# Optimization experiments

Measured on AMD Instinct MI355X. Metric: run time of the kernel, lower is better.

The kernel has to match this reference:

```python
import jax, jax.numpy as jnp
import numpy as np

EMB = 768
NH = 12
DH = EMB // NH
NORM = float(np.sqrt(DH))  # 8.0


def setup_inputs() -> dict:
    key = jax.random.key(0)
    ks = jax.random.split(key, 9)
    B, S = 1, 4096
    s = 0.02  # realistic init scale for weights
    return {
        "x": jax.random.normal(ks[0], (B, S, EMB), jnp.float32),
        "mask": jnp.ones((B, S), jnp.float32),
        "Wq": jax.random.normal(ks[1], (EMB, EMB), jnp.float32) * s,
        "bq": jnp.zeros((EMB,), jnp.float32),
        "Wk": jax.random.normal(ks[2], (EMB, EMB), jnp.float32) * s,
        "bk": jnp.zeros((EMB,), jnp.float32),
        "Wv": jax.random.normal(ks[3], (EMB, EMB), jnp.float32) * s,
        "bv": jnp.zeros((EMB,), jnp.float32),
        "Wo": jax.random.normal(ks[4], (EMB, EMB), jnp.float32) * s,
        "bo": jnp.zeros((EMB,), jnp.float32),
    }


def reference(x, mask, Wq, bq, Wk, bk, Wv, bv, Wo, bo):
    B, S, _ = x.shape
    # QKV projections (torch Linear: x @ W.T + b)
    q = x @ Wq.T + bq
    k = x @ Wk.T + bk
    v = x @ Wv.T + bv
    # split heads: b s (nh dh) -> b nh s dh
    split = lambda t: t.reshape(B, S, NH, DH).transpose(0, 2, 1, 3)
    qh, kh, vh = split(q), split(k), split(v)
    # attention scores [b, nh, s, s]
    scores = jnp.einsum("bhqd,bhkd->bhqk", qh, kh) / NORM
    # additive mask: scores -= 10000 * (1 - mask), mask broadcast over query dim
    scores = scores - 10000.0 * (1.0 - mask[:, None, None, :])
    attn = jax.nn.softmax(scores, axis=-1)
    out = jnp.einsum("bhqk,bhkd->bhqd", attn, vh)
    # b nh s dh -> b s (nh dh)
    out = out.transpose(0, 2, 1, 3).reshape(B, S, EMB)
    return out @ Wo.T + bo
```

## Files before the change

kernel.cpp:

```cpp
#include <hip/hip_runtime.h>
#include <stdint.h>
#include <stddef.h>

#define EMB 768
#define SEQ 4096
#define NH 12
#define DH 64
#define LOG2E 1.44269504f
#define NSP 2
#define SPLEN (SEQ / NSP)
#define NBLK (NH * 32 * NSP)

typedef __attribute__((ext_vector_type(8))) short short8;
typedef __attribute__((ext_vector_type(4))) float f32x4;
typedef __attribute__((ext_vector_type(16))) float f32x16;
typedef __attribute__((ext_vector_type(2))) unsigned int uint32x2;

static __device__ __forceinline__ unsigned short f2bf(float f) {
  union { float f; uint32_t u; } v; v.f = f;
  uint32_t u = v.u;
  return (unsigned short)((u + 0x7FFFu + ((u >> 16) & 1u)) >> 16);
}
static __device__ __forceinline__ float bf2f(unsigned short s) {
  union { uint32_t u; float f; } v; v.u = ((uint32_t)s) << 16;
  return v.f;
}

static __device__ __forceinline__ void gl_lds16(const void* g, void* l) {
  __builtin_amdgcn_global_load_lds(
      (const __attribute__((address_space(1))) uint32_t*)g,
      (__attribute__((address_space(3))) uint32_t*)l, 16, 0, 0);
}
static __device__ __forceinline__ void gl_lds4(const void* g, void* l) {
  __builtin_amdgcn_global_load_lds(
      (const __attribute__((address_space(1))) uint32_t*)g,
      (__attribute__((address_space(3))) uint32_t*)l, 4, 0, 0);
}

__global__ void prep_kernel(const float* __restrict__ x, const float* __restrict__ mask,
                            const float* __restrict__ Wq, const float* __restrict__ Wk,
                            const float* __restrict__ Wv, const float* __restrict__ Wo,
                            unsigned short* __restrict__ xb, unsigned short* __restrict__ wqb,
                            unsigned short* __restrict__ wkb, unsigned short* __restrict__ wvb,
                            unsigned short* __restrict__ wob, float* __restrict__ mb2) {
  const int y = blockIdx.y;
  if (y == 5) {
    int i = blockIdx.x * 256 + threadIdx.x;
    if (i < SEQ) mb2[i] = -80000.f * (1.f - mask[i]);
    return;
  }
  const float* in = y == 0 ? x : y == 1 ? Wq : y == 2 ? Wk : y == 3 ? Wv : Wo;
  unsigned short* out = y == 0 ? xb : y == 1 ? wqb : y == 2 ? wkb : y == 3 ? wvb : wob;
  const int n = (y == 0) ? SEQ * EMB : EMB * EMB;
  int stride = gridDim.x * blockDim.x * 4;
  for (int i = (blockIdx.x * blockDim.x + threadIdx.x) * 4; i < n; i += stride) {
    float4 v = *reinterpret_cast<const float4*>(in + i);
    ushort4 o;
    o.x = f2bf(v.x); o.y = f2bf(v.y); o.z = f2bf(v.z); o.w = f2bf(v.w);
    *reinterpret_cast<ushort4*>(out + i) = o;
  }
}

__global__ void norm1_kernel(const unsigned short* __restrict__ Qb,
                             const unsigned short* __restrict__ Kb,
                             float* __restrict__ pbnd) {
  const int mh = blockIdx.x;
  const int mat = mh / NH;
  const int head = mh % NH;
  const unsigned short* base = (mat == 0 ? Qb : Kb) + head * DH;
  const int t = threadIdx.x;
  const int slot = t & 7;
  const int rloc = t >> 3;
  float mx = 0.f;
#pragma unroll
  for (int p = 0; p < 4; ++p) {
    int row = blockIdx.y * 128 + p * 32 + rloc;
    short8 v = *reinterpret_cast<const short8*>(base + (size_t)row * EMB + slot * 8);
    float s = 0.f;
#pragma unroll
    for (int j = 0; j < 8; ++j) {
      float f = bf2f((unsigned short)v[j]);
      s = fmaf(f, f, s);
    }
#pragma unroll
    for (int off = 1; off < 8; off <<= 1)
      s += __shfl_xor(s, off, 64);
    mx = fmaxf(mx, s);
  }
#pragma unroll
  for (int off = 8; off < 64; off <<= 1)
    mx = fmaxf(mx, __shfl_xor(mx, off, 64));
  __shared__ float wmax[4];
  if ((t & 63) == 0) wmax[t >> 6] = mx;
  __syncthreads();
  if (t == 0)
    pbnd[mh * 32 + blockIdx.y] =
        fmaxf(fmaxf(wmax[0], wmax[1]), fmaxf(wmax[2], wmax[3]));
}

__global__ void norm2_kernel(const float* __restrict__ pbnd,
                             unsigned int* __restrict__ bnd) {
  int i = threadIdx.x;
  if (i < 2 * NH) {
    float m = 0.f;
#pragma unroll
    for (int c = 0; c < 32; ++c) m = fmaxf(m, pbnd[i * 32 + c]);
    bnd[i] = __float_as_uint(sqrtf(m));
  }
}

__global__ void lw_kernel(const float* __restrict__ lpart, float* __restrict__ cbuf) {
  int i = blockIdx.x * 256 + threadIdx.x;
  float l0 = lpart[i], l1 = lpart[i + NH * SEQ];
  cbuf[i] = l0 / (l0 + l1);
}

template <int OUT_F32>
static __device__ __forceinline__ void gemm64(
    const unsigned short* __restrict__ A, const unsigned short* __restrict__ W,
    const float* __restrict__ bias, void* __restrict__ Cout,
    int M, int N, int K, int bm, int bn) {
  __shared__ unsigned short Alds[64 * 64];
  __shared__ unsigned short Blds[128 * 64];
  const int t = threadIdx.x;
  const int lane = t & 63;
  const int wave = t >> 6;
  const int wr = wave >> 1, wc = wave & 1;
  const int lm = lane & 15, lg = lane >> 4;

  f32x4 acc[2][4];
#pragma unroll
  for (int i = 0; i < 2; ++i)
#pragma unroll
    for (int j = 0; j < 4; ++j) acc[i][j] = (f32x4){0.f, 0.f, 0.f, 0.f};

  const int srow = t >> 3;
  const int scsw = (t & 7) * 16;

  const int nK = K >> 6;
  for (int kt = 0; kt < nK; ++kt) {
    const int k0 = kt << 6;
#pragma unroll
    for (int i = 0; i < 2; ++i) {
      int row = i * 32 + srow;
      int cb = scsw ^ ((row & 7) << 4);
      gl_lds16(A + (size_t)(bm * 64 + row) * K + k0 + (cb >> 1),
               (char*)Alds + i * 4096 + t * 16);
    }
#pragma unroll
    for (int i = 0; i < 4; ++i) {
      int row = i * 32 + srow;
      int cb = scsw ^ ((row & 7) << 4);
      gl_lds16(W + (size_t)(bn * 128 + row) * K + k0 + (cb >> 1),
               (char*)Blds + i * 4096 + t * 16);
    }
    __syncthreads();
#pragma unroll
    for (int kk = 0; kk < 2; ++kk) {
      short8 af[2], bfr[4];
#pragma unroll
      for (int i = 0; i < 2; ++i) {
        int rowa = wr * 32 + i * 16 + lm;
        int cba = (kk * 64 + lg * 16) ^ ((rowa & 7) << 4);
        af[i] = *reinterpret_cast<const short8*>((const char*)Alds + rowa * 128 + cba);
      }
#pragma unroll
      for (int j = 0; j < 4; ++j) {
        int rowb = wc * 64 + j * 16 + lm;
        int cbb = (kk * 64 + lg * 16) ^ ((rowb & 7) << 4);
        bfr[j] = *reinterpret_cast<const short8*>((const char*)Blds + rowb * 128 + cbb);
      }
#pragma unroll
      for (int i = 0; i < 2; ++i)
#pragma unroll
        for (int j = 0; j < 4; ++j)
          acc[i][j] = __builtin_amdgcn_mfma_f32_16x16x32_bf16(af[i], bfr[j], acc[i][j], 0, 0, 0);
    }
    __syncthreads();
  }
#pragma unroll
  for (int i = 0; i < 2; ++i) {
    int row0 = bm * 64 + wr * 32 + i * 16 + lg * 4;
#pragma unroll
    for (int j = 0; j < 4; ++j) {
      int col = bn * 128 + wc * 64 + j * 16 + lm;
      float b = bias[col];
#pragma unroll
      for (int r = 0; r < 4; ++r) {
        float v = acc[i][j][r] + b;
        if (OUT_F32)
          ((float*)Cout)[(size_t)(row0 + r) * N + col] = v;
        else
          ((unsigned short*)Cout)[(size_t)(row0 + r) * N + col] = f2bf(v);
      }
    }
  }
}

__global__ __launch_bounds__(256, 2) void qkv_gemm(
    const unsigned short* __restrict__ A,
    const unsigned short* __restrict__ W0, const unsigned short* __restrict__ W1,
    const unsigned short* __restrict__ W2,
    const float* __restrict__ b0, const float* __restrict__ b1, const float* __restrict__ b2,
    unsigned short* __restrict__ O0, unsigned short* __restrict__ O1,
    unsigned short* __restrict__ O2) {
  const int z = blockIdx.z;
  const unsigned short* W = z == 0 ? W0 : z == 1 ? W1 : W2;
  const float* bias = z == 0 ? b0 : z == 1 ? b1 : b2;
  unsigned short* O = z == 0 ? O0 : z == 1 ? O1 : O2;
  gemm64<0>(A, W, bias, O, SEQ, EMB, EMB, blockIdx.x, blockIdx.y);
}

__global__ __launch_bounds__(256, 2) void gemm_wo_fused(
    const unsigned short* __restrict__ opart, const float* __restrict__ cbuf,
    const unsigned short* __restrict__ W, const float* __restrict__ bias,
    float* __restrict__ C) {
  __shared__ unsigned short Alds[64 * 64];
  __shared__ unsigned short Blds[128 * 64];
  const int t = threadIdx.x;
  const int lane = t & 63;
  const int wave = t >> 6;
  const int wr = wave >> 1, wc = wave & 1;
  const int lm = lane & 15, lg = lane >> 4;
  const int bm = blockIdx.x, bn = blockIdx.y;

  f32x4 acc[2][4];
#pragma unroll
  for (int i = 0; i < 2; ++i)
#pragma unroll
    for (int j = 0; j < 4; ++j) acc[i][j] = (f32x4){0.f, 0.f, 0.f, 0.f};

  const int srow = t >> 3;
  const int scsw = (t & 7) * 16;

  const int nK = EMB >> 6;
  for (int kt = 0; kt < nK; ++kt) {
    const int k0 = kt << 6;
#pragma unroll
    for (int i = 0; i < 2; ++i) {
      int row = i * 32 + srow;
      int q = bm * 64 + row;
      int cb = scsw ^ ((row & 7) << 4);
      int d = cb >> 1;
      float c0 = cbuf[kt * SEQ + q];
      float c1 = 1.f - c0;
      size_t ob = ((size_t)kt * SEQ + q) * 64 + d;
      short8 o0 = *reinterpret_cast<const short8*>(opart + ob);
      short8 o1 = *reinterpret_cast<const short8*>(opart + (size_t)NH * SEQ * 64 + ob);
      short8 m;
#pragma unroll
      for (int e = 0; e < 8; ++e)
        m[e] = (short)f2bf(c0 * bf2f((unsigned short)o0[e]) +
                           c1 * bf2f((unsigned short)o1[e]));
      *reinterpret_cast<short8*>((char*)Alds + i * 4096 + t * 16) = m;
    }
#pragma unroll
    for (int i = 0; i < 4; ++i) {
      int row = i * 32 + srow;
      int cb = scsw ^ ((row & 7) << 4);
      gl_lds16(W + (size_t)(bn * 128 + row) * EMB + k0 + (cb >> 1),
               (char*)Blds + i * 4096 + t * 16);
    }
    __syncthreads();
#pragma unroll
    for (int kk = 0; kk < 2; ++kk) {
      short8 af[2], bfr[4];
#pragma unroll
      for (int i = 0; i < 2; ++i) {
        int rowa = wr * 32 + i * 16 + lm;
        int cba = (kk * 64 + lg * 16) ^ ((rowa & 7) << 4);
        af[i] = *reinterpret_cast<const short8*>((const char*)Alds + rowa * 128 + cba);
      }
#pragma unroll
      for (int j = 0; j < 4; ++j) {
        int rowb = wc * 64 + j * 16 + lm;
        int cbb = (kk * 64 + lg * 16) ^ ((rowb & 7) << 4);
        bfr[j] = *reinterpret_cast<const short8*>((const char*)Blds + rowb * 128 + cbb);
      }
#pragma unroll
      for (int i = 0; i < 2; ++i)
#pragma unroll
        for (int j = 0; j < 4; ++j)
          acc[i][j] = __builtin_amdgcn_mfma_f32_16x16x32_bf16(af[i], bfr[j], acc[i][j], 0, 0, 0);
    }
    __syncthreads();
  }
#pragma unroll
  for (int i = 0; i < 2; ++i) {
    int row0 = bm * 64 + wr * 32 + i * 16 + lg * 4;
#pragma unroll
    for (int j = 0; j < 4; ++j) {
      int col = bn * 128 + wc * 64 + j * 16 + lm;
      float b = bias[col];
#pragma unroll
      for (int r = 0; r < 4; ++r)
        C[(size_t)(row0 + r) * EMB + col] = acc[i][j][r] + b;
    }
  }
}

__global__ void transpose_kernel(const unsigned short* __restrict__ in,
                                 unsigned short* __restrict__ out) {
  __shared__ unsigned short tile[32][33];
  int tx = threadIdx.x, ty = threadIdx.y;
  int e0 = blockIdx.x * 32, s0 = blockIdx.y * 32;
#pragma unroll
  for (int i = 0; i < 4; ++i)
    tile[ty + i * 8][tx] = in[(size_t)(s0 + ty + i * 8) * EMB + e0 + tx];
  __syncthreads();
#pragma unroll
  for (int i = 0; i < 4; ++i)
    out[(size_t)(e0 + ty + i * 8) * SEQ + s0 + tx] = tile[tx][ty + i * 8];
}

__global__ __launch_bounds__(256, 3) void attn_kernel(
    const unsigned short* __restrict__ Q, const unsigned short* __restrict__ Kb,
    const unsigned short* __restrict__ Vt, const float* __restrict__ mb2,
    const unsigned int* __restrict__ bnd,
    unsigned short* __restrict__ opart, float* __restrict__ lpart) {
  __shared__ unsigned short Klds[2][64 * DH];
  __shared__ unsigned short Vlds[2][DH * 64];
  __shared__ __align__(16) float msk[2][64];

  const int t = threadIdx.x;
  const int lane = t & 63;
  const int wave = t >> 6;
  const int o = blockIdx.x;
  const int wg = (o & 7) * (NBLK / 8) + (o >> 3);
  const int head = wg >> 6;
  const int rem = wg & 63;
  const int qb = rem >> 1;
  const int sp = rem & 1;
  const int q0 = qb * 128 + wave * 32;
  const int kvb0 = sp * SPLEN;
  const int lm = lane & 31;
  const int h = lane >> 5;

  const float sc2 = 0.125f * LOG2E;
  union { unsigned int u; float f; } qn, kn;
  qn.u = bnd[head]; kn.u = bnd[NH + head];
  const float mfix = qn.f * kn.f * sc2;

  short8 qf[4];
#pragma unroll
  for (int ks = 0; ks < 4; ++ks)
    qf[ks] = *reinterpret_cast<const short8*>(
        Q + (size_t)(q0 + lm) * EMB + head * DH + ks * 16 + h * 8);

  short8 ones;
#pragma unroll
  for (int i = 0; i < 8; ++i) ones[i] = (short)0x3F80;

  f32x16 oacc[2], lacc;
#pragma unroll
  for (int n = 0; n < 2; ++n)
#pragma unroll
    for (int r = 0; r < 16; ++r) oacc[n][r] = 0.f;
#pragma unroll
  for (int r = 0; r < 16; ++r) lacc[r] = 0.f;

  const int srow = t >> 3;
  const int scol = (t & 7) * 16;

  auto STAGE = [&](int buf, int kt2) {
    const int kv0 = kvb0 + kt2 * 64;
#pragma unroll
    for (int i = 0; i < 2; ++i) {
      int row = i * 32 + srow;
      int cb = scol ^ ((row & 7) << 4);
      gl_lds16(Kb + (size_t)(kv0 + row) * EMB + head * DH + (cb >> 1),
               (char*)Klds + buf * 8192 + i * 4096 + t * 16);
      gl_lds16(Vt + (size_t)(head * DH + row) * SEQ + kv0 + (cb >> 1),
               (char*)Vlds + buf * 8192 + i * 4096 + t * 16);
    }
    gl_lds4(mb2 + kv0 + lane, &msk[buf][0]);
  };

  constexpr int NT = SPLEN / 64;
  STAGE(0, 0);
  __syncthreads();

  for (int kt = 0; kt < NT; ++kt) {
    const int buf = kt & 1;
    if (kt + 1 < NT) STAGE(buf ^ 1, kt + 1);

    f32x16 s[2];
#pragma unroll
    for (int tt = 0; tt < 2; ++tt)
#pragma unroll
      for (int a = 0; a < 4; ++a) {
        f32x4 m = *reinterpret_cast<const f32x4*>(&msk[buf][tt * 32 + a * 8 + h * 4]);
#pragma unroll
        for (int i = 0; i < 4; ++i) s[tt][a * 4 + i] = m[i];
      }

    __builtin_amdgcn_s_setprio(1);
#pragma unroll
    for (int tt = 0; tt < 2; ++tt)
#pragma unroll
      for (int ks = 0; ks < 4; ++ks) {
        int row = tt * 32 + lm;
        int cb = (ks * 32 + h * 16) ^ ((row & 7) << 4);
        short8 kf = *reinterpret_cast<const short8*>(
            (const char*)Klds + buf * 8192 + row * 128 + cb);
        s[tt] = __builtin_amdgcn_mfma_f32_32x32x16_bf16(kf, qf[ks], s[tt], 0, 0, 0);
      }
    __builtin_amdgcn_s_setprio(0);

#pragma unroll
    for (int tt = 0; tt < 2; ++tt)
#pragma unroll
      for (int r = 0; r < 16; ++r)
        s[tt][r] = __builtin_amdgcn_exp2f(fmaf(s[tt][r], sc2, -mfix));

    short8 pa[4];
#pragma unroll
    for (int tt = 0; tt < 2; ++tt) {
      uint32_t r0[4], r1[4];
#pragma unroll
      for (int a = 0; a < 4; ++a) {
        asm("v_cvt_pk_bf16_f32 %0, %1, %2" : "=v"(r0[a]) : "v"(s[tt][4 * a]), "v"(s[tt][4 * a + 1]));
        asm("v_cvt_pk_bf16_f32 %0, %1, %2" : "=v"(r1[a]) : "v"(s[tt][4 * a + 2]), "v"(s[tt][4 * a + 3]));
      }
#pragma unroll
      for (int ksl = 0; ksl < 2; ++ksl) {
        uint32x2 w0 = __builtin_amdgcn_permlane32_swap(r0[2 * ksl], r0[2 * ksl + 1], false, false);
        uint32x2 w1 = __builtin_amdgcn_permlane32_swap(r1[2 * ksl], r1[2 * ksl + 1], false, false);
        union { short8 s8; uint32_t u[4]; } pk;
        pk.u[0] = w0[0]; pk.u[1] = w1[0]; pk.u[2] = w0[1]; pk.u[3] = w1[1];
        pa[tt * 2 + ksl] = pk.s8;
      }
    }

    __builtin_amdgcn_s_setprio(1);
#pragma unroll
    for (int n = 0; n < 2; ++n)
#pragma unroll
      for (int ks = 0; ks < 4; ++ks) {
        int row = n * 32 + lm;
        int cb = (ks * 32 + h * 16) ^ ((row & 7) << 4);
        short8 vf = *reinterpret_cast<const short8*>(
            (const char*)Vlds + buf * 8192 + row * 128 + cb);
        oacc[n] = __builtin_amdgcn_mfma_f32_32x32x16_bf16(pa[ks], vf, oacc[n], 0, 0, 0);
      }
#pragma unroll
    for (int ks = 0; ks < 4; ++ks)
      lacc = __builtin_amdgcn_mfma_f32_32x32x16_bf16(pa[ks], ones, lacc, 0, 0, 0);
    __builtin_amdgcn_s_setprio(0);

    __syncthreads();
  }

  f32x16 rl;
#pragma unroll
  for (int r = 0; r < 16; ++r) rl[r] = __builtin_amdgcn_rcpf(lacc[r]);
  unsigned short* ob = opart + ((size_t)(sp * NH + head) * SEQ + q0) * 64;
#pragma unroll
  for (int n = 0; n < 2; ++n)
#pragma unroll
    for (int r = 0; r < 16; ++r) {
      int crow = (r & 3) + 8 * (r >> 2) + 4 * h;
      ob[crow * 64 + n * 32 + lm] = f2bf(oacc[n][r] * rl[r]);
    }
  const size_t pbase = (size_t)(sp * NH + head) * SEQ + q0;
  if (lm == 0) {
#pragma unroll
    for (int r = 0; r < 16; ++r) {
      int crow = (r & 3) + 8 * (r >> 2) + 4 * h;
      lpart[pbase + crow] = lacc[r];
    }
  }
}

extern "C" void kernel_launch(void* const* d_in, const int* in_sizes, int n_in,
                              void* d_out, int out_size, void* d_ws, size_t ws_size,
                              hipStream_t stream) {
  const float* x    = (const float*)d_in[0];
  const float* mask = (const float*)d_in[1];
  const float* Wq   = (const float*)d_in[2];
  const float* bq   = (const float*)d_in[3];
  const float* Wk   = (const float*)d_in[4];
  const float* bk   = (const float*)d_in[5];
  const float* Wv   = (const float*)d_in[6];
  const float* bv   = (const float*)d_in[7];
  const float* Wo   = (const float*)d_in[8];
  const float* bo   = (const float*)d_in[9];
  float* out = (float*)d_out;

  char* ws = (char*)d_ws;
  const size_t SZ_X = (size_t)SEQ * EMB * 2;
  const size_t SZ_W = (size_t)EMB * EMB * 2;
  unsigned short* xb  = (unsigned short*)(ws);
  unsigned short* wqb = (unsigned short*)(ws + SZ_X);
  unsigned short* wkb = (unsigned short*)(ws + SZ_X + SZ_W);
  unsigned short* wvb = (unsigned short*)(ws + SZ_X + 2 * SZ_W);
  unsigned short* wob = (unsigned short*)(ws + SZ_X + 3 * SZ_W);
  unsigned short* Qb  = (unsigned short*)(ws + SZ_X + 4 * SZ_W);
  unsigned short* Kbuf= (unsigned short*)(ws + 2 * SZ_X + 4 * SZ_W);
  unsigned short* Vb  = (unsigned short*)(ws + 3 * SZ_X + 4 * SZ_W);
  unsigned short* Vtb = (unsigned short*)(ws + 4 * SZ_X + 4 * SZ_W);
  size_t off = 5 * SZ_X + 4 * SZ_W;
  float* mb2            = (float*)(ws + off);          off += (size_t)SEQ * 4;
  unsigned short* opart = (unsigned short*)(ws + off); off += (size_t)NSP * NH * SEQ * 64 * 2;
  float* lpart          = (float*)(ws + off);          off += (size_t)NSP * NH * SEQ * 4;
  unsigned int* bnd     = (unsigned int*)(ws + off);   off += 256;
  float* pbnd           = (float*)(ws + off);          off += 1024;
  float* cbuf           = (float*)(ws + off);

  prep_kernel<<<dim3(192, 6), 256, 0, stream>>>(
      x, mask, Wq, Wk, Wv, Wo, xb, wqb, wkb, wvb, wob, mb2);

  qkv_gemm<<<dim3(SEQ / 64, EMB / 128, 3), 256, 0, stream>>>(
      xb, wqb, wkb, wvb, bq, bk, bv, Qb, Kbuf, Vb);

  norm1_kernel<<<dim3(2 * NH, 32), 256, 0, stream>>>(Qb, Kbuf, pbnd);
  norm2_kernel<<<1, 64, 0, stream>>>(pbnd, bnd);

  transpose_kernel<<<dim3(EMB / 32, SEQ / 32), dim3(32, 8), 0, stream>>>(Vb, Vtb);

  attn_kernel<<<NBLK, 256, 0, stream>>>(Qb, Kbuf, Vtb, mb2, bnd, opart, lpart);

  lw_kernel<<<NH * SEQ / 256, 256, 0, stream>>>(lpart, cbuf);

  gemm_wo_fused<<<dim3(SEQ / 64, EMB / 128), 256, 0, stream>>>(
      opart, cbuf, wob, bo, out);
}
```

Measured before the change: 134.0 us.

## Fuse V transpose into QKV GEMM epilogue and move split merge before Wo GEMM

The QKV GEMM now writes V already transposed, staging the tile through shared memory, so the separate transpose kernel is removed. The split-sequence partial outputs are merged by a dedicated merge kernel into a bf16 activation buffer. The Wo projection then runs as a plain GEMM with direct global-to-LDS loads, replacing the fused merge-in-load path and the lw kernel. This trades one extra pass over the merged output for a simpler, async-loaded GEMM and fewer launches.

After: 125.2 us (median of 2 runs). 6.6% less time.

```diff
diff --git a/kernel.cpp b/kernel.cpp
--- a/kernel.cpp
+++ b/kernel.cpp
@@ -12,6 +12,7 @@
 #define NBLK (NH * 32 * NSP)
 
 typedef __attribute__((ext_vector_type(8))) short short8;
+typedef __attribute__((ext_vector_type(4))) short short4v;
 typedef __attribute__((ext_vector_type(4))) float f32x4;
 typedef __attribute__((ext_vector_type(16))) float f32x16;
 typedef __attribute__((ext_vector_type(2))) unsigned int uint32x2;
@@ -107,12 +108,6 @@
     for (int c = 0; c < 32; ++c) m = fmaxf(m, pbnd[i * 32 + c]);
     bnd[i] = __float_as_uint(sqrtf(m));
   }
-}
-
-__global__ void lw_kernel(const float* __restrict__ lpart, float* __restrict__ cbuf) {
-  int i = blockIdx.x * 256 + threadIdx.x;
-  float l0 = lpart[i], l1 = lpart[i + NH * SEQ];
-  cbuf[i] = l0 / (l0 + l1);
 }
 
 template <int OUT_F32>
@@ -197,32 +192,33 @@
   }
 }
 
+__global__ __launch_bounds__(256, 2) void gemm_wo(
+    const unsigned short* __restrict__ A, const unsigned short* __restrict__ W,
+    const float* __restrict__ bias, float* __restrict__ C) {
+  gemm64<1>(A, W, bias, C, SEQ, EMB, EMB, blockIdx.x, blockIdx.y);
+}
+
 __global__ __launch_bounds__(256, 2) void qkv_gemm(
     const unsigned short* __restrict__ A,
     const unsigned short* __restrict__ W0, const unsigned short* __restrict__ W1,
     const unsigned short* __restrict__ W2,
     const float* __restrict__ b0, const float* __restrict__ b1, const float* __restrict__ b2,
-    unsigned short* __restrict__ O0, unsigned short* __restrict__ O1,
-    unsigned short* __restrict__ O2) {
+    unsigned short* __restrict__ Qo, unsigned short* __restrict__ Ko,
+    unsigned short* __restrict__ Vto) {
+  __shared__ unsigned short smem[12288];
+  unsigned short* Alds = smem;
+  unsigned short* Blds = smem + 4096;
+
   const int z = blockIdx.z;
   const unsigned short* W = z == 0 ? W0 : z == 1 ? W1 : W2;
   const float* bias = z == 0 ? b0 : z == 1 ? b1 : b2;
-  unsigned short* O = z == 0 ? O0 : z == 1 ? O1 : O2;
-  gemm64<0>(A, W, bias, O, SEQ, EMB, EMB, blockIdx.x, blockIdx.y);
-}
-
-__global__ __launch_bounds__(256, 2) void gemm_wo_fused(
-    const unsigned short* __restrict__ opart, const float* __restrict__ cbuf,
-    const unsigned short* __restrict__ W, const float* __restrict__ bias,
-    float* __restrict__ C) {
-  __shared__ unsigned short Alds[64 * 64];
-  __shared__ unsigned short Blds[128 * 64];
+  const int bm = blockIdx.x, bn = blockIdx.y;
+
   const int t = threadIdx.x;
   const int lane = t & 63;
   const int wave = t >> 6;
   const int wr = wave >> 1, wc = wave & 1;
   const int lm = lane & 15, lg = lane >> 4;
-  const int bm = blockIdx.x, bn = blockIdx.y;
 
   f32x4 acc[2][4];
 #pragma unroll
@@ -233,26 +229,14 @@
   const int srow = t >> 3;
   const int scsw = (t & 7) * 16;
 
-  const int nK = EMB >> 6;
-  for (int kt = 0; kt < nK; ++kt) {
+  for (int kt = 0; kt < EMB / 64; ++kt) {
     const int k0 = kt << 6;
 #pragma unroll
     for (int i = 0; i < 2; ++i) {
       int row = i * 32 + srow;
-      int q = bm * 64 + row;
       int cb = scsw ^ ((row & 7) << 4);
-      int d = cb >> 1;
-      float c0 = cbuf[kt * SEQ + q];
-      float c1 = 1.f - c0;
-      size_t ob = ((size_t)kt * SEQ + q) * 64 + d;
-      short8 o0 = *reinterpret_cast<const short8*>(opart + ob);
-      short8 o1 = *reinterpret_cast<const short8*>(opart + (size_t)NH * SEQ * 64 + ob);
-      short8 m;
-#pragma unroll
-      for (int e = 0; e < 8; ++e)
-        m[e] = (short)f2bf(c0 * bf2f((unsigned short)o0[e]) +
-                           c1 * bf2f((unsigned short)o1[e]));
-      *reinterpret_cast<short8*>((char*)Alds + i * 4096 + t * 16) = m;
+      gl_lds16(A + (size_t)(bm * 64 + row) * EMB + k0 + (cb >> 1),
+               (char*)Alds + i * 4096 + t * 16);
     }
 #pragma unroll
     for (int i = 0; i < 4; ++i) {
@@ -285,32 +269,46 @@
     }
     __syncthreads();
   }
-#pragma unroll
-  for (int i = 0; i < 2; ++i) {
-    int row0 = bm * 64 + wr * 32 + i * 16 + lg * 4;
-#pragma unroll
-    for (int j = 0; j < 4; ++j) {
-      int col = bn * 128 + wc * 64 + j * 16 + lm;
-      float b = bias[col];
-#pragma unroll
-      for (int r = 0; r < 4; ++r)
-        C[(size_t)(row0 + r) * EMB + col] = acc[i][j][r] + b;
-    }
-  }
-}
-
-__global__ void transpose_kernel(const unsigned short* __restrict__ in,
-                                 unsigned short* __restrict__ out) {
-  __shared__ unsigned short tile[32][33];
-  int tx = threadIdx.x, ty = threadIdx.y;
-  int e0 = blockIdx.x * 32, s0 = blockIdx.y * 32;
-#pragma unroll
-  for (int i = 0; i < 4; ++i)
-    tile[ty + i * 8][tx] = in[(size_t)(s0 + ty + i * 8) * EMB + e0 + tx];
-  __syncthreads();
-#pragma unroll
-  for (int i = 0; i < 4; ++i)
-    out[(size_t)(e0 + ty + i * 8) * SEQ + s0 + tx] = tile[tx][ty + i * 8];
+
+  if (z < 2) {
+    unsigned short* O = z == 0 ? Qo : Ko;
+#pragma unroll
+    for (int i = 0; i < 2; ++i) {
+      int row0 = bm * 64 + wr * 32 + i * 16 + lg * 4;
+#pragma unroll
+      for (int j = 0; j < 4; ++j) {
+        int col = bn * 128 + wc * 64 + j * 16 + lm;
+        float b = bias[col];
+#pragma unroll
+        for (int r = 0; r < 4; ++r)
+          O[(size_t)(row0 + r) * EMB + col] = f2bf(acc[i][j][r] + b);
+      }
+    }
+  } else {
+    unsigned short* T = smem;
+#pragma unroll
+    for (int i = 0; i < 2; ++i) {
+      int rowL = wr * 32 + i * 16 + lg * 4;
+#pragma unroll
+      for (int j = 0; j < 4; ++j) {
+        int colL = wc * 64 + j * 16 + lm;
+        float b = bias[bn * 128 + colL];
+        short4v s4;
+#pragma unroll
+        for (int r = 0; r < 4; ++r) s4[r] = (short)f2bf(acc[i][j][r] + b);
+        *reinterpret_cast<short4v*>(T + colL * 72 + rowL) = s4;
+      }
+    }
+    __syncthreads();
+#pragma unroll
+    for (int p = 0; p < 4; ++p) {
+      int col = p * 32 + (t >> 3);
+      int chunk = (t & 7) * 8;
+      short8 v = *reinterpret_cast<const short8*>(T + col * 72 + chunk);
+      *reinterpret_cast<short8*>(
+          Vto + (size_t)(bn * 128 + col) * SEQ + bm * 64 + chunk) = v;
+    }
+  }
 }
 
 __global__ __launch_bounds__(256, 3) void attn_kernel(
@@ -470,6 +468,31 @@
       lpart[pbase + crow] = lacc[r];
     }
   }
+}
+
+__global__ void merge_kernel(const unsigned short* __restrict__ opart,
+                             const float* __restrict__ lpart,
+                             unsigned short* __restrict__ Ab) {
+  int tid = blockIdx.x * 256 + threadIdx.x;
+  int dv = tid & 15;
+  int rq = tid >> 4;
+  int head = rq >> 12;
+  int q = rq & 4095;
+  size_t base = (size_t)head * SEQ + q;
+  const size_t str = (size_t)NH * SEQ;
+
+  float l0 = lpart[base], l1 = lpart[base + str];
+  float rd = 1.0f / (l0 + l1);
+  float c0 = l0 * rd, c1 = l1 * rd;
+
+  ushort4 o0 = *reinterpret_cast<const ushort4*>(opart + base * 64 + dv * 4);
+  ushort4 o1 = *reinterpret_cast<const ushort4*>(opart + (base + str) * 64 + dv * 4);
+  ushort4 r;
+  r.x = f2bf(c0 * bf2f(o0.x) + c1 * bf2f(o1.x));
+  r.y = f2bf(c0 * bf2f(o0.y) + c1 * bf2f(o1.y));
+  r.z = f2bf(c0 * bf2f(o0.z) + c1 * bf2f(o1.z));
+  r.w = f2bf(c0 * bf2f(o0.w) + c1 * bf2f(o1.w));
+  *reinterpret_cast<ushort4*>(Ab + (size_t)q * EMB + head * DH + dv * 4) = r;
 }
 
 extern "C" void kernel_launch(void* const* d_in, const int* in_sizes, int n_in,
@@ -497,31 +520,27 @@
   unsigned short* wob = (unsigned short*)(ws + SZ_X + 3 * SZ_W);
   unsigned short* Qb  = (unsigned short*)(ws + SZ_X + 4 * SZ_W);
   unsigned short* Kbuf= (unsigned short*)(ws + 2 * SZ_X + 4 * SZ_W);
-  unsigned short* Vb  = (unsigned short*)(ws + 3 * SZ_X + 4 * SZ_W);
-  unsigned short* Vtb = (unsigned short*)(ws + 4 * SZ_X + 4 * SZ_W);
+  unsigned short* Vtb = (unsigned short*)(ws + 3 * SZ_X + 4 * SZ_W);
+  unsigned short* Ab  = (unsigned short*)(ws + 4 * SZ_X + 4 * SZ_W);
   size_t off = 5 * SZ_X + 4 * SZ_W;
   float* mb2            = (float*)(ws + off);          off += (size_t)SEQ * 4;
   unsigned short* opart = (unsigned short*)(ws + off); off += (size_t)NSP * NH * SEQ * 64 * 2;
   float* lpart          = (float*)(ws + off);          off += (size_t)NSP * NH * SEQ * 4;
   unsigned int* bnd     = (unsigned int*)(ws + off);   off += 256;
-  float* pbnd           = (float*)(ws + off);          off += 1024;
-  float* cbuf           = (float*)(ws + off);
+  float* pbnd           = (float*)(ws + off);
 
   prep_kernel<<<dim3(192, 6), 256, 0, stream>>>(
       x, mask, Wq, Wk, Wv, Wo, xb, wqb, wkb, wvb, wob, mb2);
 
   qkv_gemm<<<dim3(SEQ / 64, EMB / 128, 3), 256, 0, stream>>>(
-      xb, wqb, wkb, wvb, bq, bk, bv, Qb, Kbuf, Vb);
+      xb, wqb, wkb, wvb, bq, bk, bv, Qb, Kbuf, Vtb);
 
   norm1_kernel<<<dim3(2 * NH, 32), 256, 0, stream>>>(Qb, Kbuf, pbnd);
   norm2_kernel<<<1, 64, 0, stream>>>(pbnd, bnd);
 
-  transpose_kernel<<<dim3(EMB / 32, SEQ / 32), dim3(32, 8), 0, stream>>>(Vb, Vtb);
-
   attn_kernel<<<NBLK, 256, 0, stream>>>(Qb, Kbuf, Vtb, mb2, bnd, opart, lpart);
 
-  lw_kernel<<<NH * SEQ / 256, 256, 0, stream>>>(lpart, cbuf);
-
-  gemm_wo_fused<<<dim3(SEQ / 64, EMB / 128), 256, 0, stream>>>(
-      opart, cbuf, wob, bo, out);
-}
+  merge_kernel<<<3072, 256, 0, stream>>>(opart, lpart, Ab);
+
+  gemm_wo<<<dim3(SEQ / 64, EMB / 128), 256, 0, stream>>>(Ab, wob, bo, out);
+}
```
